# Kernel optimization log

Hardware: AMD Instinct MI355X
Metric: run time of the kernel (lower is better)

The kernel has to match this reference:

```python
import jax, jax.numpy as jnp
import numpy as np

H = 4    # heads
DK = 5   # d_k = d_model // h = 20 // 4
D = 20   # d_model


def _proj(x, W, b):
    # x: [B,S,D] -> [B,H,S,DK]
    B, S, _ = x.shape
    y = x @ W.T + b
    return y.reshape(B, S, H, DK).transpose(0, 2, 1, 3)


def _attn(q, k, v, mask4):
    # q,k,v: [B,H,S,DK]; mask4: [B,1,1,S]
    scores = jnp.einsum('bhqd,bhkd->bhqk', q, k) / jnp.sqrt(jnp.asarray(DK, q.dtype))
    scores = jnp.where(mask4 == 0, jnp.asarray(-1e9, q.dtype), scores)
    p = jax.nn.softmax(scores, axis=-1)  # dropout omitted (eval mode)
    return jnp.einsum('bhqk,bhkd->bhqd', p, v)


def setup_inputs() -> dict:
    key = jax.random.key(0)
    ks = jax.random.split(key, 12)
    B, S = 8, 2048
    scale = 1.0 / np.sqrt(D)
    inp = {
        'query': jax.random.normal(ks[0], (B, S, D), dtype=jnp.float32),
        'key': jax.random.normal(ks[1], (B, S, D), dtype=jnp.float32),
        'value': jax.random.normal(ks[2], (B, S, D), dtype=jnp.float32),
        'mask': jax.random.randint(ks[3], (B, S), 0, 2, dtype=jnp.int32),
    }
    for i in range(4):
        inp[f'W{i}'] = jax.random.normal(ks[4 + 2 * i], (D, D), dtype=jnp.float32) * scale
        inp[f'b{i}'] = jax.random.normal(ks[5 + 2 * i], (D,), dtype=jnp.float32) * 0.01
    return inp


def reference(query, key, value, mask, W0, b0, W1, b1, W2, b2, W3, b3):
    B, S, _ = query.shape
    mask4 = mask[:, None, None, :]  # [B,1,1,S]
    # Six permuted (arg-to-linear0, arg-to-linear1, arg-to-linear2) variants,
    # exactly as the torch forward: (q,k,k),(k,q,q),(q,v,v),(v,q,q),(k,v,v),(v,k,k)
    triples = [
        (query, key, key), (key, query, query),
        (query, value, value), (value, query, query),
        (key, value, value), (value, key, key),
    ]
    out = None
    for a, bb, c in triples:
        o = _attn(_proj(a, W0, b0), _proj(bb, W1, b1), _proj(c, W2, b2), mask4)
        out = o if out is None else out + o
    # merge heads: [B,H,S,DK] -> [B,S,D]
    out = out.transpose(0, 2, 1, 3).reshape(B, S, H * DK)
    return out @ W3.T + b3
```

## Files before the change

### kernel.cpp

```cpp
#include <hip/hip_runtime.h>
#include <cstdint>
#include <cstddef>

#define B    8
#define SEQ  2048
#define H    4
#define DKN  5
#define DIM  20
#define PRE8 8
#define SENTB ((short)0xC2FC)
#define ONEB  ((short)0x3F80)
#define B128  ((short)0x4300)
#define PBIASM 12599162.0f

typedef short short8 __attribute__((ext_vector_type(8)));
typedef float f32x16 __attribute__((ext_vector_type(16)));

static __device__ __forceinline__ unsigned short bf16b(float x) {
    union { float f; unsigned u; } v; v.f = x;
    unsigned r = v.u + 0x7FFFu + ((v.u >> 16) & 1u);
    return (unsigned short)(r >> 16);
}
static __device__ __forceinline__ float bf16f(unsigned short h) {
    union { unsigned u; float f; } v; v.u = ((unsigned)h) << 16;
    return v.f;
}
static __device__ __forceinline__ unsigned pk_pbits(float ta, float tb) {
    unsigned ia, ib;
    __builtin_memcpy(&ia, &ta, 4);
    __builtin_memcpy(&ib, &tb, 4);
    return __builtin_amdgcn_perm(ib, ia, 0x05040100u);
}
static __device__ __forceinline__ int sig32(int t) {
    return (t & 19) | ((t & 4) << 1) | ((t & 8) >> 1);
}

typedef unsigned __attribute__((address_space(1))) gas_u32;
typedef unsigned __attribute__((address_space(3))) las_u32;
static __device__ __forceinline__ void glds16(const void* g, void* l) {
    __builtin_amdgcn_global_load_lds((const gas_u32*)g, (las_u32*)l, 16, 0, 0);
}


__global__ __launch_bounds__(256) void proj_kernel(
    const float* __restrict__ q, const float* __restrict__ k, const float* __restrict__ v,
    const float* __restrict__ W0, const float* __restrict__ b0,
    const float* __restrict__ W1, const float* __restrict__ b1,
    const float* __restrict__ W2, const float* __restrict__ b2,
    const int* __restrict__ mask,
    short* __restrict__ Qt, short* __restrict__ Kt, short* __restrict__ Vt,
    int* __restrict__ meta)
{
    __shared__ float Ws[3][DIM * DIM];
    __shared__ float bsh[3][DIM];
    __shared__ int   widx[256];
    __shared__ int   cntS;

    int tid = threadIdx.x;
    int blk = blockIdx.x;
    int w   = blk & 7;  blk >>= 3;
    int h   = blk & 3;  blk >>= 2;
    int bb  = blk & 7;  blk >>= 3;
    int x   = blk;
    int s0  = w * 256;

    for (int i = tid; i < DIM * DIM; i += 256) {
        Ws[0][i] = W0[i]; Ws[1][i] = W1[i]; Ws[2][i] = W2[i];
    }
    if (tid < DIM) { bsh[0][tid] = b0[tid]; bsh[1][tid] = b1[tid]; bsh[2][tid] = b2[tid]; }

    if (tid < 64) {
        const int* mrow = mask + bb * SEQ;
        int base = 0;
        for (int ch = 0; ch < SEQ; ch += 64) {
            int mv = mrow[ch + tid];
            unsigned long long bal = __ballot(mv != 0);
            int pos = base + (int)__popcll(bal & ((1ull << tid) - 1ull));
            if (mv && pos >= s0 && pos < s0 + 256) widx[pos - s0] = ch + tid;
            base += (int)__popcll(bal);
        }
        if (tid == 0) {
            cntS = base;
            if (x == 0 && h == 0 && w == 0) meta[bb] = base;
        }
    }
    __syncthreads();

    int  cnt   = cntS;
    int  c     = s0 + tid;
    bool valid = c < cnt;
    int  gs    = valid ? widx[tid] : 0;

    const float QSC = 0.44721359549995793f * 1.4426950408889634f * 128.0f;
    const float* base = (x == 0) ? q : ((x == 1) ? k : v);

    float xq[DIM], xg[DIM];
    {
        const float4* r4 = (const float4*)(base + (size_t)(bb * SEQ + c) * DIM);
        const float4* g4 = (const float4*)(base + (size_t)(bb * SEQ + gs) * DIM);
        #pragma unroll
        for (int i = 0; i < 5; ++i) {
            float4 a = r4[i], g = g4[i];
            xq[i*4+0]=a.x; xq[i*4+1]=a.y; xq[i*4+2]=a.z; xq[i*4+3]=a.w;
            xg[i*4+0]=g.x; xg[i*4+1]=g.y; xg[i*4+2]=g.z; xg[i*4+3]=g.w;
        }
    }

    #define DOT20(xv, t, j, dst) {                                        \
        float acc_ = bsh[t][j];                                           \
        const float4* wr_ = (const float4*)&Ws[t][(j) * DIM];             \
        _Pragma("unroll")                                                 \
        for (int i4 = 0; i4 < 5; ++i4) {                                  \
            float4 w_ = wr_[i4];                                          \
            acc_ += (xv)[i4*4+0]*w_.x + (xv)[i4*4+1]*w_.y                 \
                  + (xv)[i4*4+2]*w_.z + (xv)[i4*4+3]*w_.w;                \
        }                                                                 \
        dst = acc_;                                                       \
    }

    size_t row = ((size_t)(x * B + bb) * H + h) * SEQ + c;

    short8 qhi = {0, 0, 0, 0, 0, B128, 0, 0};
    short8 qlo = {0, 0, 0, 0, 0, 0, 0, 0};
    #pragma unroll
    for (int d = 0; d < DKN; ++d) {
        float y; DOT20(xq, 0, h * DKN + d, y);
        y *= QSC;
        unsigned short hb = bf16b(y);
        qhi[d] = (short)hb;
        qlo[d] = (short)bf16b(y - bf16f(hb));
    }
    ((short8*)Qt)[row * 2 + 0] = qhi;
    ((short8*)Qt)[row * 2 + 1] = qlo;

    short8 rk = {0, 0, 0, 0, 0, valid ? (short)0 : SENTB, 0, 0};
    if (valid) {
        #pragma unroll
        for (int d = 0; d < DKN; ++d) {
            float y; DOT20(xg, 1, h * DKN + d, y);
            rk[d] = (short)bf16b(y);
        }
    }
    ((short8*)Kt)[row] = rk;

    if (valid) {
        size_t vb = ((size_t)(x * B + bb) * H + h) * 8 * SEQ;
        size_t vcell = vb + (size_t)(c >> 5) * 256 + sig32(c & 31);
        #pragma unroll
        for (int d = 0; d < DKN; ++d) {
            float y; DOT20(xg, 2, h * DKN + d, y);
            Vt[vcell + (size_t)d * 32] = (short)bf16b(y);
        }
        Vt[vcell + (size_t)5 * 32] = ONEB;
    }
}

__global__ __launch_bounds__(128, 3) void attn_kernel(
    const short* __restrict__ Qt, const short* __restrict__ Kt,
    const short* __restrict__ Vt, const int* __restrict__ meta,
    float* __restrict__ pre)
{
    __shared__ char lds[2][4][2048];

    int wv   = threadIdx.x >> 6;
    int lane = threadIdx.x & 63;
    int l31  = lane & 31, half = lane >> 5;

    int wid  = blockIdx.x;
    int qtq  = wid / 96;
    int grp  = wid - qtq * 96;
    int h    = grp & 3;  grp >>= 2;
    int b    = grp & 7;  grp >>= 3;
    int kvi  = grp;
    int aA = (0x001 >> (4 * kvi)) & 0xF;
    int aB = (0x122 >> (4 * kvi)) & 0xF;
    int pA = (0x201 >> (4 * kvi)) & 0xF;
    int pB = (0x453 >> (4 * kvi)) & 0xF;
    int qt0  = qtq * 4 + wv * 2;

    int cnt  = meta[b];
    int kend = (cnt + 63) & ~63;

    const short* QbA = Qt + ((size_t)(aA * B + b) * H + h) * SEQ * 16;
    const short* QbB = Qt + ((size_t)(aB * B + b) * H + h) * SEQ * 16;
    const char*  Kst = (const char*)(Kt + ((size_t)(kvi * B + b) * H + h) * SEQ * 8);
    const char*  Vst = (const char*)(Vt + ((size_t)(kvi * B + b) * H + h) * 8 * SEQ);

    char* myl = &lds[wv][0][0];
    int koff = l31 * 16;
    int voff = 1024 + (l31 & 7) * 64 + half * 16;

    short8 qf[2][2];
    f32x16 acc[2][2];
    f32x16 zc = {0.f,0.f,0.f,0.f,0.f,0.f,0.f,0.f,0.f,0.f,0.f,0.f,0.f,0.f,0.f,0.f};
    f32x16 sb = {PBIASM,PBIASM,PBIASM,PBIASM,PBIASM,PBIASM,PBIASM,PBIASM,
                 PBIASM,PBIASM,PBIASM,PBIASM,PBIASM,PBIASM,PBIASM,PBIASM};
    #pragma unroll
    for (int t = 0; t < 2; ++t) {
        size_t qrow = (size_t)((qt0 + t) * 32 + l31) * 16 + half * 8;
        qf[0][t] = *(const short8*)(QbA + qrow);
        qf[1][t] = *(const short8*)(QbB + qrow);
        acc[0][t] = zc;
        acc[1][t] = zc;
    }
    asm volatile("s_waitcnt vmcnt(0)" ::: "memory");
    __builtin_amdgcn_sched_barrier(0);

    #pragma unroll
    for (int j = 0; j < 3; ++j) {
        char* nb = myl + (j << 11);
        size_t ob = ((size_t)j << 10) + lane * 16;
        glds16(Kst + ob, nb);
        glds16(Vst + ob, nb + 1024);
    }

    #define PVSTEP(D, VA, VC, ACC) {                                          \
        unsigned p0_[4], p1_[4];                                              \
        _Pragma("unroll")                                                     \
        for (int r = 0; r < 4; ++r) {                                         \
            p0_[r] = pk_pbits(D[2 * r],     D[2 * r + 1]);                    \
            p1_[r] = pk_pbits(D[2 * r + 8], D[2 * r + 9]);                    \
        }                                                                     \
        short8 f0_, f1_;                                                      \
        __builtin_memcpy(&f0_, p0_, 16);                                      \
        __builtin_memcpy(&f1_, p1_, 16);                                      \
        ACC = __builtin_amdgcn_mfma_f32_32x32x16_bf16(VA, f0_, ACC, 0, 0, 0); \
        ACC = __builtin_amdgcn_mfma_f32_32x32x16_bf16(VC, f1_, ACC, 0, 0, 0); \
    }

    int NT = kend >> 6;
    for (int i = 0; i < NT; ++i) {
        {
            size_t ob = ((size_t)(i + 3) << 10) + lane * 16;
            char* nb = myl + (((i + 3) & 3) << 11);
            glds16(Kst + ob, nb);
            glds16(Vst + ob, nb + 1024);
        }

        __builtin_amdgcn_sched_barrier(0);
        asm volatile("s_waitcnt vmcnt(6)" ::: "memory");
        __builtin_amdgcn_sched_barrier(0);

        const char* cb = myl + ((i & 3) << 11);
        short8 kfA = *(const short8*)(cb + koff);
        short8 vaA = *(const short8*)(cb + voff);
        short8 vcA = *(const short8*)(cb + voff + 32);

        __builtin_amdgcn_s_setprio(1);
        #pragma unroll
        for (int pr = 0; pr < 2; ++pr) {
            #pragma unroll
            for (int t = 0; t < 2; ++t) {
                f32x16 dA = __builtin_amdgcn_mfma_f32_32x32x16_bf16(
                    kfA, qf[pr][t], sb, 0, 0, 0);
                PVSTEP(dA, vaA, vcA, acc[pr][t]);
            }
        }
        __builtin_amdgcn_s_setprio(0);

        short8 kfB = *(const short8*)(cb + koff + 512);
        short8 vaB = *(const short8*)(cb + voff + 512);
        short8 vcB = *(const short8*)(cb + voff + 544);

        __builtin_amdgcn_s_setprio(1);
        #pragma unroll
        for (int pr = 0; pr < 2; ++pr) {
            #pragma unroll
            for (int t = 0; t < 2; ++t) {
                f32x16 dB = __builtin_amdgcn_mfma_f32_32x32x16_bf16(
                    kfB, qf[pr][t], sb, 0, 0, 0);
                PVSTEP(dB, vaB, vcB, acc[pr][t]);
            }
        }
        __builtin_amdgcn_s_setprio(0);
    }

    #pragma unroll
    for (int pr = 0; pr < 2; ++pr) {
        int p = pr ? pB : pA;
        float* base0 = pre + (((size_t)p * B + b) * H + h) * SEQ * PRE8;
        #pragma unroll
        for (int t = 0; t < 2; ++t) {
            int qb = (qt0 + t) * 32;
            float lv  = __shfl(acc[pr][t][1], 32 + l31, 64);
            float inv = 1.0f / lv;
            float* dst = base0 + (size_t)(qb + l31) * PRE8;
            if (half == 0)
                *(float4*)dst = make_float4(acc[pr][t][0]*inv, acc[pr][t][1]*inv,
                                            acc[pr][t][2]*inv, acc[pr][t][3]*inv);
            else
                dst[4] = acc[pr][t][0] * inv;
        }
    }
}

__global__ __launch_bounds__(64) void final_kernel(
    const float* __restrict__ pre,
    const float* __restrict__ W3, const float* __restrict__ b3,
    float* __restrict__ out)
{
    __shared__ float Ws[DIM * DIM];
    __shared__ float bs[DIM];
    int tid = threadIdx.x;
    for (int i = tid; i < DIM * DIM; i += 64) Ws[i] = W3[i];
    if (tid < DIM) bs[tid] = b3[tid];
    __syncthreads();

    int g = blockIdx.x * 64 + tid;
    int b = g / SEQ;
    int s = g - b * SEQ;

    float x[DIM];
    #pragma unroll
    for (int i = 0; i < DIM; ++i) x[i] = 0.f;

    for (int p = 0; p < 6; ++p) {
        #pragma unroll
        for (int h = 0; h < H; ++h) {
            const float* sr = pre + (((size_t)p * B + b) * H + h) * SEQ * PRE8
                                  + (size_t)s * PRE8;
            float4 a = *(const float4*)sr;
            float  a4 = sr[4];
            x[h * DKN + 0] += a.x; x[h * DKN + 1] += a.y; x[h * DKN + 2] += a.z;
            x[h * DKN + 3] += a.w; x[h * DKN + 4] += a4;
        }
    }

    float y[DIM];
    for (int j = 0; j < DIM; ++j) {
        float acc = bs[j];
        const float4* wr = (const float4*)&Ws[j * DIM];
        #pragma unroll
        for (int i4 = 0; i4 < 5; ++i4) {
            float4 w = wr[i4];
            acc += x[i4*4+0]*w.x + x[i4*4+1]*w.y + x[i4*4+2]*w.z + x[i4*4+3]*w.w;
        }
        y[j] = acc;
    }
    float4* dst = (float4*)(out + (size_t)(b * SEQ + s) * DIM);
    #pragma unroll
    for (int j4 = 0; j4 < 5; ++j4)
        dst[j4] = make_float4(y[j4*4+0], y[j4*4+1], y[j4*4+2], y[j4*4+3]);
}

extern "C" void kernel_launch(void* const* d_in, const int* in_sizes, int n_in,
                              void* d_out, int out_size, void* d_ws, size_t ws_size,
                              hipStream_t stream) {
    const float* q    = (const float*)d_in[0];
    const float* k    = (const float*)d_in[1];
    const float* v    = (const float*)d_in[2];
    const int*   mask = (const int*)d_in[3];
    const float* W0 = (const float*)d_in[4];  const float* b0 = (const float*)d_in[5];
    const float* W1 = (const float*)d_in[6];  const float* b1 = (const float*)d_in[7];
    const float* W2 = (const float*)d_in[8];  const float* b2 = (const float*)d_in[9];
    const float* W3 = (const float*)d_in[10]; const float* b3 = (const float*)d_in[11];

    const size_t NROW = (size_t)3 * B * H * SEQ;
    short* Qt = (short*)d_ws;
    short* Kt = Qt + NROW * 16;
    short* Vt = Kt + NROW * 8;
    float* pre = (float*)(Vt + NROW * 8);
    int*   meta = (int*)(pre + (size_t)6 * B * H * SEQ * PRE8);
    float* out = (float*)d_out;

    proj_kernel<<<dim3(3 * B * H * (SEQ / 256)), dim3(256), 0, stream>>>(
        q, k, v, W0, b0, W1, b1, W2, b2, mask, Qt, Kt, Vt, meta);
    attn_kernel<<<dim3(3 * B * H * 16), dim3(128), 0, stream>>>(
        Qt, Kt, Vt, meta, pre);
    final_kernel<<<dim3(B * SEQ / 64), dim3(64), 0, stream>>>(pre, W3, b3, out);
}
```

Measured before the change: 138.2 us.

## Software-pipeline QK and PV MFMAs across half-tiles in attention loop

Restructures the attention inner loop so the PV MFMAs for the previous half-tile's probabilities are issued together with the QK MFMAs and probability packing for the current half-tile. A prologue computes the first half-tile's probabilities and an epilogue drains the final PV step. The goal is to hide the QK-to-exp-to-PV dependency latency and keep the matrix units busy. The change also lowers launch-bounds occupancy from 3 to 2 to free registers for the extra live probability fragments, which risks reduced latency hiding across waves. The global-to-LDS prefetch is now skipped on the last iteration, and the wait count is changed.

Result: no change. 138.6 us (+0.3%).

```diff
diff --git a/kernel.cpp b/kernel.cpp
--- a/kernel.cpp
+++ b/kernel.cpp
@@ -155,7 +155,7 @@
     }
 }
 
-__global__ __launch_bounds__(128, 3) void attn_kernel(
+__global__ __launch_bounds__(128, 2) void attn_kernel(
     const short* __restrict__ Qt, const short* __restrict__ Kt,
     const short* __restrict__ Vt, const int* __restrict__ meta,
     float* __restrict__ pre)
@@ -214,65 +214,94 @@
         glds16(Vst + ob, nb + 1024);
     }
 
-    #define PVSTEP(D, VA, VC, ACC) {                                          \
-        unsigned p0_[4], p1_[4];                                              \
+    #define QKM(KF, QF) __builtin_amdgcn_mfma_f32_32x32x16_bf16((KF), (QF), sb, 0, 0, 0)
+    #define PGEN(D, PA, PB_) {                                                \
+        unsigned q0_[4], q1_[4];                                              \
         _Pragma("unroll")                                                     \
         for (int r = 0; r < 4; ++r) {                                         \
-            p0_[r] = pk_pbits(D[2 * r],     D[2 * r + 1]);                    \
-            p1_[r] = pk_pbits(D[2 * r + 8], D[2 * r + 9]);                    \
+            q0_[r] = pk_pbits((D)[2 * r],     (D)[2 * r + 1]);                \
+            q1_[r] = pk_pbits((D)[2 * r + 8], (D)[2 * r + 9]);                \
         }                                                                     \
-        short8 f0_, f1_;                                                      \
-        __builtin_memcpy(&f0_, p0_, 16);                                      \
-        __builtin_memcpy(&f1_, p1_, 16);                                      \
-        ACC = __builtin_amdgcn_mfma_f32_32x32x16_bf16(VA, f0_, ACC, 0, 0, 0); \
-        ACC = __builtin_amdgcn_mfma_f32_32x32x16_bf16(VC, f1_, ACC, 0, 0, 0); \
+        __builtin_memcpy(&(PA), q0_, 16);                                     \
+        __builtin_memcpy(&(PB_), q1_, 16);                                    \
+    }
+    #define SUBSTEP(KF, VA, VC) {                                             \
+        acc[0][0] = __builtin_amdgcn_mfma_f32_32x32x16_bf16(vaP, ppa[0][0], acc[0][0], 0, 0, 0); \
+        acc[0][0] = __builtin_amdgcn_mfma_f32_32x32x16_bf16(vcP, ppb[0][0], acc[0][0], 0, 0, 0); \
+        acc[0][1] = __builtin_amdgcn_mfma_f32_32x32x16_bf16(vaP, ppa[0][1], acc[0][1], 0, 0, 0); \
+        acc[0][1] = __builtin_amdgcn_mfma_f32_32x32x16_bf16(vcP, ppb[0][1], acc[0][1], 0, 0, 0); \
+        acc[1][0] = __builtin_amdgcn_mfma_f32_32x32x16_bf16(vaP, ppa[1][0], acc[1][0], 0, 0, 0); \
+        acc[1][0] = __builtin_amdgcn_mfma_f32_32x32x16_bf16(vcP, ppb[1][0], acc[1][0], 0, 0, 0); \
+        acc[1][1] = __builtin_amdgcn_mfma_f32_32x32x16_bf16(vaP, ppa[1][1], acc[1][1], 0, 0, 0); \
+        acc[1][1] = __builtin_amdgcn_mfma_f32_32x32x16_bf16(vcP, ppb[1][1], acc[1][1], 0, 0, 0); \
+        f32x16 d00 = QKM(KF, qf[0][0]);                                       \
+        f32x16 d01 = QKM(KF, qf[0][1]);                                       \
+        PGEN(d00, ppa[0][0], ppb[0][0]);                                      \
+        f32x16 d10 = QKM(KF, qf[1][0]);                                       \
+        PGEN(d01, ppa[0][1], ppb[0][1]);                                      \
+        f32x16 d11 = QKM(KF, qf[1][1]);                                       \
+        PGEN(d10, ppa[1][0], ppb[1][0]);                                      \
+        PGEN(d11, ppa[1][1], ppb[1][1]);                                      \
+        vaP = VA; vcP = VC;                                                   \
+    }
+
+    short8 ppa[2][2], ppb[2][2];
+    short8 vaP, vcP;
+
+    __builtin_amdgcn_sched_barrier(0);
+    asm volatile("s_waitcnt vmcnt(4)" ::: "memory");
+    __builtin_amdgcn_sched_barrier(0);
+    {
+        short8 kf0 = *(const short8*)(myl + koff);
+        vaP = *(const short8*)(myl + voff);
+        vcP = *(const short8*)(myl + voff + 32);
+        f32x16 d00 = QKM(kf0, qf[0][0]);
+        f32x16 d01 = QKM(kf0, qf[0][1]);
+        PGEN(d00, ppa[0][0], ppb[0][0]);
+        f32x16 d10 = QKM(kf0, qf[1][0]);
+        PGEN(d01, ppa[0][1], ppb[0][1]);
+        f32x16 d11 = QKM(kf0, qf[1][1]);
+        PGEN(d10, ppa[1][0], ppb[1][0]);
+        PGEN(d11, ppa[1][1], ppb[1][1]);
     }
 
     int NT = kend >> 6;
     for (int i = 0; i < NT; ++i) {
-        {
+        const char* cb = myl + ((i & 3) << 11);
+        short8 kfB = *(const short8*)(cb + koff + 512);
+        short8 vaB = *(const short8*)(cb + voff + 512);
+        short8 vcB = *(const short8*)(cb + voff + 544);
+        __builtin_amdgcn_s_setprio(1);
+        SUBSTEP(kfB, vaB, vcB);
+        __builtin_amdgcn_s_setprio(0);
+
+        if (i + 1 < NT) {
             size_t ob = ((size_t)(i + 3) << 10) + lane * 16;
             char* nb = myl + (((i + 3) & 3) << 11);
             glds16(Kst + ob, nb);
             glds16(Vst + ob, nb + 1024);
-        }
-
-        __builtin_amdgcn_sched_barrier(0);
-        asm volatile("s_waitcnt vmcnt(6)" ::: "memory");
-        __builtin_amdgcn_sched_barrier(0);
-
-        const char* cb = myl + ((i & 3) << 11);
-        short8 kfA = *(const short8*)(cb + koff);
-        short8 vaA = *(const short8*)(cb + voff);
-        short8 vcA = *(const short8*)(cb + voff + 32);
-
-        __builtin_amdgcn_s_setprio(1);
-        #pragma unroll
-        for (int pr = 0; pr < 2; ++pr) {
-            #pragma unroll
-            for (int t = 0; t < 2; ++t) {
-                f32x16 dA = __builtin_amdgcn_mfma_f32_32x32x16_bf16(
-                    kfA, qf[pr][t], sb, 0, 0, 0);
-                PVSTEP(dA, vaA, vcA, acc[pr][t]);
-            }
-        }
-        __builtin_amdgcn_s_setprio(0);
-
-        short8 kfB = *(const short8*)(cb + koff + 512);
-        short8 vaB = *(const short8*)(cb + voff + 512);
-        short8 vcB = *(const short8*)(cb + voff + 544);
-
-        __builtin_amdgcn_s_setprio(1);
-        #pragma unroll
-        for (int pr = 0; pr < 2; ++pr) {
-            #pragma unroll
-            for (int t = 0; t < 2; ++t) {
-                f32x16 dB = __builtin_amdgcn_mfma_f32_32x32x16_bf16(
-                    kfB, qf[pr][t], sb, 0, 0, 0);
-                PVSTEP(dB, vaB, vcB, acc[pr][t]);
-            }
-        }
-        __builtin_amdgcn_s_setprio(0);
+
+            __builtin_amdgcn_sched_barrier(0);
+            asm volatile("s_waitcnt vmcnt(4)" ::: "memory");
+            __builtin_amdgcn_sched_barrier(0);
+
+            const char* cb1 = myl + (((i + 1) & 3) << 11);
+            short8 kfA = *(const short8*)(cb1 + koff);
+            short8 vaA = *(const short8*)(cb1 + voff);
+            short8 vcA = *(const short8*)(cb1 + voff + 32);
+            __builtin_amdgcn_s_setprio(1);
+            SUBSTEP(kfA, vaA, vcA);
+            __builtin_amdgcn_s_setprio(0);
+        }
+    }
+
+    #pragma unroll
+    for (int pr = 0; pr < 2; ++pr) {
+        #pragma unroll
+        for (int t = 0; t < 2; ++t) {
+            acc[pr][t] = __builtin_amdgcn_mfma_f32_32x32x16_bf16(vaP, ppa[pr][t], acc[pr][t], 0, 0, 0);
+            acc[pr][t] = __builtin_amdgcn_mfma_f32_32x32x16_bf16(vcP, ppb[pr][t], acc[pr][t], 0, 0, 0);
+        }
     }
 
     #pragma unroll
```
